# Kernel optimization log

Hardware: AMD Instinct MI355X
Metric: run time of the kernel (lower is better)

## Reference

```python
import jax, jax.numpy as jnp
import numpy as np

EPS = 1e-5

def _bn(x, s, b, m, v):
    # inference-mode BatchNorm2d over channel axis of NCHW
    return (x - m[None, :, None, None]) * jax.lax.rsqrt(v[None, :, None, None] + EPS) \
           * s[None, :, None, None] + b[None, :, None, None]

def _conv3(x, w):
    return jax.lax.conv_general_dilated(x, w, (1, 1), 'SAME',
                                        dimension_numbers=('NCHW', 'OIHW', 'NCHW'))

def _conv1(x, w, b):
    # 1x1 conv as einsum; w: [out_c, in_c]
    return jnp.einsum('oc,bchw->bohw', w, x) + b[None, :, None, None]

def _cca(f, qw, qb, kw, kb, vw, vb, gamma):
    # Criss-cross attention (faithful to source: no diagonal -inf masking, INF() unused there)
    B, C, H, W = f.shape
    q = _conv1(f, qw, qb)   # [B, C/8, H, W]
    k = _conv1(f, kw, kb)   # [B, C/8, H, W]
    v = _conv1(f, vw, vb)   # [B, C,   H, W]
    # energy along column (same w, all h') and row (same h, all w')
    eH = jnp.einsum('bchw,bciw->bhwi', q, k)            # [B,H,W,H]
    eW = jnp.einsum('bchw,bchj->bhwj', q, k)            # [B,H,W,W]
    att = jax.nn.softmax(jnp.concatenate([eH, eW], axis=3), axis=3)  # [B,H,W,H+W]
    aH, aW = att[..., :H], att[..., H:]
    oH = jnp.einsum('bhwi,bciw->bchw', aH, v)
    oW = jnp.einsum('bhwj,bchj->bchw', aW, v)
    return gamma * (oH + oW) + f


def setup_inputs() -> dict:
    key = jax.random.key(0)
    ks = iter(jax.random.split(key, 64))
    B, Cin, H, W = 8, 2048, 64, 64
    Ci, Cq, Co = 256, 32, 512
    rn = lambda s, sc=0.02: jax.random.normal(next(ks), s, jnp.float32) * sc
    ru = lambda s: jax.random.uniform(next(ks), s, jnp.float32)
    return {
        'x': jax.random.normal(next(ks), (B, Cin, H, W), jnp.float32),
        'recurrence': 2,
        'conva_w': rn((Ci, Cin, 3, 3)),
        'bn_a_s': ru((Ci,)), 'bn_a_b': rn((Ci,), 0.1), 'bn_a_m': rn((Ci,), 0.1), 'bn_a_v': ru((Ci,)),
        'q_w': rn((Cq, Ci)), 'q_b': rn((Cq,), 0.1),
        'k_w': rn((Cq, Ci)), 'k_b': rn((Cq,), 0.1),
        'v_w': rn((Ci, Ci)), 'v_b': rn((Ci,), 0.1),
        'cca_gamma': rn((1,), 1.0),
        'convb_w': rn((Ci, Ci, 3, 3)),
        'bn_b_s': ru((Ci,)), 'bn_b_b': rn((Ci,), 0.1), 'bn_b_m': rn((Ci,), 0.1), 'bn_b_v': ru((Ci,)),
        'sq_w': rn((Ci, Ci)), 'sq_b': rn((Ci,), 0.1),
        'bn_g_s': ru((Ci,)), 'bn_g_b': rn((Ci,), 0.1), 'bn_g_m': rn((Ci,), 0.1), 'bn_g_v': ru((Ci,)),
        'fc1_w': rn((Ci // 2, Ci)), 'fc1_b': rn((Ci // 2,), 0.1),
        'fc2_w': rn((Ci, Ci // 2)), 'fc2_b': rn((Ci,), 0.1),
        'bott_w': rn((Co, Cin + 2 * Ci, 3, 3)),
        'bn_t_s': ru((Co,)), 'bn_t_b': rn((Co,), 0.1), 'bn_t_m': rn((Co,), 0.1), 'bn_t_v': ru((Co,)),
    }


def reference(x, recurrence, conva_w, bn_a_s, bn_a_b, bn_a_m, bn_a_v,
              q_w, q_b, k_w, k_b, v_w, v_b, cca_gamma,
              convb_w, bn_b_s, bn_b_b, bn_b_m, bn_b_v,
              sq_w, sq_b, bn_g_s, bn_g_b, bn_g_m, bn_g_v,
              fc1_w, fc1_b, fc2_w, fc2_b,
              bott_w, bn_t_s, bn_t_b, bn_t_m, bn_t_v):
    out = _bn(_conv3(x, conva_w), bn_a_s, bn_a_b, bn_a_m, bn_a_v)
    # Global_Avg_Pooling (SE gating) on conva output
    fm = jax.nn.relu(_bn(_conv1(out, sq_w, sq_b), bn_g_s, bn_g_b, bn_g_m, bn_g_v))
    vec = fm.mean(axis=(-2, -1))                       # [B, Ci]
    h = jax.nn.relu(vec @ fc1_w.T + fc1_b)
    gate = jax.nn.sigmoid(h @ fc2_w.T + fc2_b)
    out_gap = out * gate[:, :, None, None]
    # recurrent criss-cross attention
    for _ in range(recurrence):
        out = _cca(out, q_w, q_b, k_w, k_b, v_w, v_b, cca_gamma)
    out = _bn(_conv3(out, convb_w), bn_b_s, bn_b_b, bn_b_m, bn_b_v)
    cat = jnp.concatenate([x, out, out_gap], axis=1)   # [B, Cin+2*Ci, H, W]
    return _bn(_conv3(cat, bott_w), bn_t_s, bn_t_b, bn_t_m, bn_t_v)
```

## Files before the change

kernel.cpp:

```cpp
#include <hip/hip_runtime.h>
#include <hip/hip_bf16.h>

typedef unsigned short u16;
typedef unsigned int u32;
typedef __attribute__((ext_vector_type(8))) short short8;
typedef __attribute__((ext_vector_type(8))) unsigned short u16x8;
typedef __attribute__((ext_vector_type(4))) float f32x4;

#define BN_EPS 1e-5f
#define PADW 66
#define CATC 2560

__device__ __forceinline__ u16 f2b(float f) {
    __hip_bfloat16 h = __float2bfloat16(f);
    return *reinterpret_cast<u16*>(&h);
}
__device__ __forceinline__ float b2f(u16 u) {
    __hip_bfloat16 h;
    *reinterpret_cast<u16*>(&h) = u;
    return __bfloat162float(h);
}
__device__ __forceinline__ void async_copy16(void* lds, const void* g) {
    __builtin_amdgcn_global_load_lds((const __attribute__((address_space(1))) u32*)g,
                                     (__attribute__((address_space(3))) u32*)lds, 16, 0, 0);
}
__device__ __forceinline__ void fence_() { asm volatile("" ::: "memory"); }
__device__ __forceinline__ void barrier_() { fence_(); __builtin_amdgcn_s_barrier(); fence_(); }

template<int TAPS, int BN, int EPI, int CPT, int NTILES, int KSPLIT>
__global__ __launch_bounds__(512, 2)
void gemm8(const u16* __restrict__ Ag, int cstride,
           const u16* __restrict__ Bg, int ktot_full, int klen,
           const float* __restrict__ alpha, const float* __restrict__ beta,
           u16* __restrict__ outb, int ostride, int ochoff,
           float* __restrict__ outf, int nch)
{
    constexpr int WN   = BN / 4;
    constexpr int NSUB = WN / 16;
    constexpr int NQ   = NSUB / 2;
    constexpr int BLH  = BN / 128;
    constexpr int ASZ  = 256 * 128;
    constexpr int BSZ  = BN * 128;
    const int KT = klen / 64;

    extern __shared__ __align__(16) char smem[];
    char* smA = smem;
    char* smB = smem + 2 * ASZ;

    const int tid  = threadIdx.x;
    const int lane = tid & 63;
    const int wave = tid >> 6;
    const int wr = wave >> 2;
    const int wc = wave & 3;

    const int nwg = gridDim.x;
    const int wg  = blockIdx.x;
    const int swz = (wg & 7) * (nwg >> 3) + (wg >> 3);
    const int sel = swz % (NTILES * KSPLIT);
    const int m0  = (swz / (NTILES * KSPLIT)) * 256;
    const int n0  = (sel / KSPLIT) * BN;
    const int ks  = sel % KSPLIT;
    const int kstart = ks * klen;

    const int sr = tid >> 3;
    const int sc = tid & 7;
    const int scx8 = (sc ^ (sr & 7)) * 8;
    long apix[4];
#pragma unroll
    for (int j = 0; j < 4; ++j) {
        int p = m0 + j * 64 + sr;
        int b = p >> 12, h = (p >> 6) & 63, w = p & 63;
        apix[j] = (TAPS == 1) ? ((long)(b * PADW + h + 1) * PADW + (w + 1))
                              : ((long)(b * PADW + h) * PADW + w);
    }
    long brow[2 * BLH];
#pragma unroll
    for (int h = 0; h < 2; ++h)
#pragma unroll
        for (int l = 0; l < BLH; ++l)
            brow[h * BLH + l] = (long)(n0 + h * (BN / 2) + l * 64 + sr) * ktot_full;

    auto stA = [&](int bsel, int h, int c0, long toff) {
#pragma unroll
        for (int l = 0; l < 2; ++l) {
            const u16* g = Ag + (apix[2 * h + l] + toff) * cstride + c0 + scx8;
            async_copy16(smA + bsel * ASZ + h * 16384 + l * 8192 + tid * 16, g);
        }
    };
    auto stB = [&](int bsel, int h, int k0) {
#pragma unroll
        for (int l = 0; l < BLH; ++l) {
            const u16* g = Bg + brow[h * BLH + l] + k0 + scx8;
            async_copy16(smB + bsel * BSZ + h * (BSZ / 2) + l * 8192 + tid * 16, g);
        }
    };

    const int rsel  = lane & 15;
    const int cswz0 = (((lane >> 4)     ^ (lane & 7)) << 4);
    const int cswz1 = (((4 | (lane >> 4)) ^ (lane & 7)) << 4);

    f32x4 acc[8][NSUB] = {};
    short8 a[4][2], b0[NQ][2], b1[NQ][2];

    auto ldA = [&](int bsel, int mh) {
        const char* base = smA + bsel * ASZ + (wr * 128 + mh * 64 + rsel) * 128;
#pragma unroll
        for (int mi = 0; mi < 4; ++mi) {
            a[mi][0] = *(const short8*)(base + mi * 2048 + cswz0);
            a[mi][1] = *(const short8*)(base + mi * 2048 + cswz1);
        }
    };
    auto ldB = [&](int bsel, int nh, short8 (&bb)[NQ][2]) {
        const char* base = smB + bsel * BSZ + (wc * WN + nh * (WN / 2) + rsel) * 128;
#pragma unroll
        for (int nj = 0; nj < NQ; ++nj) {
            bb[nj][0] = *(const short8*)(base + nj * 2048 + cswz0);
            bb[nj][1] = *(const short8*)(base + nj * 2048 + cswz1);
        }
    };
    auto quad = [&](int MH, int NH, short8 (&bb)[NQ][2]) {
#pragma unroll
        for (int mi = 0; mi < 4; ++mi)
#pragma unroll
            for (int nj = 0; nj < NQ; ++nj)
#pragma unroll
                for (int kk = 0; kk < 2; ++kk)
                    acc[MH * 4 + mi][NH * NQ + nj] =
                        __builtin_amdgcn_mfma_f32_16x16x32_bf16(
                            a[mi][kk], bb[nj][kk], acc[MH * 4 + mi][NH * NQ + nj], 0, 0, 0);
    };

    const int tap0 = kstart / CPT;
    int c0_ = kstart - tap0 * CPT;
    int dx_ = tap0 % 3;
    long toff_ = dx_ + (long)(tap0 / 3) * PADW;
    auto adv = [&]() {
        c0_ += 64;
        if (c0_ == CPT) { c0_ = 0; toff_ += 1; if (++dx_ == 3) { dx_ = 0; toff_ += PADW - 3; } }
    };

    stA(0, 0, c0_, toff_); stA(0, 1, c0_, toff_); stB(0, 0, kstart); stB(0, 1, kstart);
    adv();
    stB(1, 0, kstart + 64); stB(1, 1, kstart + 64); stA(1, 0, c0_, toff_); stA(1, 1, c0_, toff_);
    int pc0 = c0_; long ptoff = toff_;
    adv();
    int skb = kstart + 128;

    if constexpr (BN == 256) asm volatile("s_waitcnt vmcnt(8)" ::: "memory");
    else                     asm volatile("s_waitcnt vmcnt(6)" ::: "memory");
    barrier_();

    for (int kt = 0; kt < KT; ++kt) {
        const int buf = kt & 1;
        ldA(buf, 0); ldB(buf, 0, b0);
        if (kt >= 1 && kt + 1 < KT) stA(buf ^ 1, 1, pc0, ptoff);
        barrier_(); asm volatile("s_waitcnt lgkmcnt(0)" ::: "memory");
        __builtin_amdgcn_s_setprio(1); quad(0, 0, b0); __builtin_amdgcn_s_setprio(0);
        barrier_();
        ldB(buf, 1, b1);
        barrier_(); asm volatile("s_waitcnt lgkmcnt(0)" ::: "memory");
        __builtin_amdgcn_s_setprio(1); quad(0, 1, b1); __builtin_amdgcn_s_setprio(0);
        barrier_();
        ldA(buf, 1);
        if (kt + 2 < KT) stB(buf, 0, skb);
        barrier_(); asm volatile("s_waitcnt lgkmcnt(0)" ::: "memory");
        __builtin_amdgcn_s_setprio(1); quad(1, 0, b0); __builtin_amdgcn_s_setprio(0);
        barrier_();
        if (kt + 2 < KT) { stB(buf, 1, skb); stA(buf, 0, c0_, toff_); }
        barrier_();
        __builtin_amdgcn_s_setprio(1); quad(1, 1, b1); __builtin_amdgcn_s_setprio(0);
        if (kt + 2 >= KT) {
            asm volatile("s_waitcnt vmcnt(0)" ::: "memory");
        } else if constexpr (BN == 256) {
            asm volatile("s_waitcnt vmcnt(6)" ::: "memory");
        } else {
            asm volatile("s_waitcnt vmcnt(4)" ::: "memory");
        }
        barrier_();
        pc0 = c0_; ptoff = toff_;
        adv(); skb += 64;
    }

    const int nl = lane & 15, mq = lane >> 4;
#pragma unroll
    for (int s = 0; s < 8; ++s) {
#pragma unroll
        for (int nj = 0; nj < NSUB; ++nj) {
            int n = n0 + wc * WN + nj * 16 + nl;
            float al = (EPI == 4) ? 1.f : alpha[n];
            float be = (EPI == 4) ? 0.f : beta[n];
#pragma unroll
            for (int r = 0; r < 4; ++r) {
                int m = m0 + wr * 128 + s * 16 + mq * 4 + r;
                float v = acc[s][nj][r] * al + be;
                if (EPI == 0) {
                    int b = m >> 12, h = (m >> 6) & 63, w = m & 63;
                    long addr = ((long)(b * PADW + h + 1) * PADW + (w + 1)) * ostride + ochoff + n;
                    outb[addr] = f2b(v);
                } else if (EPI == 2) {
                    int b = m >> 12, h = (m >> 6) & 63, w = m & 63;
                    outf[((long)(b * nch + n) << 12) + (h * 64 + w)] = v;
                } else {
                    outf[(long)ks * ((long)32768 * nch) + (long)m * nch + n] = v;
                }
            }
        }
    }
}

__global__ void combine_k(const float* __restrict__ P,
                          const float* __restrict__ alpha, const float* __restrict__ beta,
                          u16* __restrict__ dst, int dstride, int choff)
{
    int m = blockIdx.x, n = threadIdx.x;
    int b = m >> 12, h = (m >> 6) & 63, w = m & 63;
    float v = P[(long)m * 256 + n] + P[(long)32768 * 256 + (long)m * 256 + n];
    v = v * alpha[n] + beta[n];
    dst[((long)(b * PADW + h + 1) * PADW + (w + 1)) * dstride + choff + n] = f2b(v);
}

template<int TAPS, int EPI>
__global__ __launch_bounds__(256, 2)
void gemm_conv(const u16* __restrict__ A, int cstride, int cpt,
               const u16* __restrict__ Bw, int ktot,
               const float* __restrict__ alpha, const float* __restrict__ beta,
               u16* __restrict__ outb, int ostride, int ochoff,
               float* __restrict__ outf, int n_total)
{
    __shared__ u16 As[128][32];
    __shared__ u16 Bs[128][32];
    __shared__ float red[128];

    const int tid  = threadIdx.x;
    const int lane = tid & 63;
    const int wave = tid >> 6;
    const int wr = wave >> 1, wc = wave & 1;
    const int m0 = blockIdx.y * 128;
    const int n0 = blockIdx.x * 128;

    long pixbase[2];
    long browk[2];
#pragma unroll
    for (int i = 0; i < 2; ++i) {
        int row = i * 64 + (tid >> 2);
        int p = m0 + row;
        int b = p >> 12, h = (p >> 6) & 63, w = p & 63;
        if (TAPS == 1) pixbase[i] = (long)(b * PADW + h + 1) * PADW + (w + 1);
        else           pixbase[i] = (long)(b * PADW + h) * PADW + w;
        browk[i] = (long)(n0 + row) * ktot;
    }
    const int chunk = (tid & 3) * 8;

    f32x4 acc[4][4] = {};

    const int steps = ktot / 32;
    int c0 = 0, dx = 0;
    long toff = 0;
    for (int s = 0; s < steps; ++s) {
        const int k0 = s * 32;
#pragma unroll
        for (int i = 0; i < 2; ++i) {
            const u16* ga = A + (pixbase[i] + ((TAPS == 1) ? 0 : toff)) * cstride + c0 + chunk;
            async_copy16((char*)(&As[0][0]) + i * 4096 + tid * 16, ga);
            const u16* gb = Bw + browk[i] + k0 + chunk;
            async_copy16((char*)(&Bs[0][0]) + i * 4096 + tid * 16, gb);
        }
        asm volatile("s_waitcnt vmcnt(0)" ::: "memory");
        __syncthreads();

        short8 af[4], bf[4];
#pragma unroll
        for (int x = 0; x < 4; ++x) {
            af[x] = *(const short8*)&As[wr * 64 + x * 16 + (lane & 15)][(lane >> 4) * 8];
            bf[x] = *(const short8*)&Bs[wc * 64 + x * 16 + (lane & 15)][(lane >> 4) * 8];
        }
#pragma unroll
        for (int mi = 0; mi < 4; ++mi)
#pragma unroll
            for (int ni = 0; ni < 4; ++ni)
                acc[mi][ni] = __builtin_amdgcn_mfma_f32_16x16x32_bf16(af[mi], bf[ni], acc[mi][ni], 0, 0, 0);
        __syncthreads();

        c0 += 32;
        if (TAPS > 1 && c0 == cpt) {
            c0 = 0; dx++; toff += 1;
            if (dx == 3) { dx = 0; toff += PADW - 3; }
        }
    }

    const int nl = lane & 15;
    const int mq = lane >> 4;

    if (EPI == 3) {
        if (tid < 128) red[tid] = 0.f;
        __syncthreads();
#pragma unroll
        for (int ni = 0; ni < 4; ++ni) {
            int ncol = wc * 64 + ni * 16 + nl;
            int n = n0 + ncol;
            float aa = alpha[n], bb = beta[n];
            float ssum = 0.f;
#pragma unroll
            for (int mi = 0; mi < 4; ++mi)
#pragma unroll
                for (int r = 0; r < 4; ++r)
                    ssum += fmaxf(acc[mi][ni][r] * aa + bb, 0.f);
            atomicAdd(&red[ncol], ssum);
        }
        __syncthreads();
        if (tid < 128) {
            int b = m0 >> 12;
            atomicAdd(&outf[b * 256 + n0 + tid], red[tid]);
        }
    } else {
#pragma unroll
        for (int mi = 0; mi < 4; ++mi) {
#pragma unroll
            for (int r = 0; r < 4; ++r) {
                int m = m0 + wr * 64 + mi * 16 + mq * 4 + r;
#pragma unroll
                for (int ni = 0; ni < 4; ++ni) {
                    int n = n0 + wc * 64 + ni * 16 + nl;
                    float v = acc[mi][ni][r] * alpha[n] + beta[n];
                    outb[(long)m * ostride + n] = f2b(v);
                }
            }
        }
    }
}

__global__ void xpad_k(const float* __restrict__ x, u16* __restrict__ cat)
{
    __shared__ float T[64][65];
    int bh = blockIdx.y;
    int b = bh >> 6, h = bh & 63;
    int c0 = blockIdx.x * 64;
    int t = threadIdx.x;
#pragma unroll
    for (int i = 0; i < 16; ++i) {
        int cl = i * 4 + (t >> 6);
        int w = t & 63;
        T[cl][w] = x[(((long)b * 2048 + c0 + cl) * 64 + h) * 64 + w];
    }
    __syncthreads();
#pragma unroll
    for (int i = 0; i < 16; ++i) {
        int wl = i * 4 + (t >> 6);
        int cl = t & 63;
        cat[((long)(b * PADW + h + 1) * PADW + (wl + 1)) * CATC + c0 + cl] = f2b(T[cl][wl]);
    }
}

__global__ void prep_w3(const float* __restrict__ w, u16* __restrict__ o, int O, int C)
{
    int idx = blockIdx.x * 256 + threadIdx.x;
    if (idx >= O * C) return;
    int oo = idx / C, c = idx - oo * C;
    const float* s = w + (long)idx * 9;
    long base = (long)oo * 9 * C + c;
#pragma unroll
    for (int t = 0; t < 9; ++t) o[base + (long)t * C] = f2b(s[t]);
}

__global__ void prep_qkv(const float* __restrict__ qw, const float* __restrict__ kw,
                         const float* __restrict__ vw, u16* __restrict__ o)
{
    int idx = blockIdx.x * 256 + threadIdx.x;
    int n = idx >> 8, c = idx & 255;
    float v;
    if (n < 32) v = qw[n * 256 + c];
    else if (n < 64) v = kw[(n - 32) * 256 + c];
    else if (n < 320) v = vw[(n - 64) * 256 + c];
    else v = 0.f;
    o[idx] = f2b(v);
}

__global__ void prep_cast(const float* __restrict__ w, u16* __restrict__ o, int n)
{
    int i = blockIdx.x * 256 + threadIdx.x;
    if (i < n) o[i] = f2b(w[i]);
}

__global__ void prep_ab(const float* as, const float* ab, const float* am, const float* av,
                        const float* gs, const float* gb, const float* gm, const float* gv, const float* sqb,
                        const float* bs, const float* bb, const float* bm, const float* bv,
                        const float* ts, const float* tb, const float* tm, const float* tv,
                        const float* qb, const float* kb, const float* vb,
                        float* Aa, float* Ba_, float* Ag, float* Bg, float* Ab2, float* Bb2,
                        float* At, float* Bt, float* Aq, float* Bq)
{
    int i = blockIdx.x * 256 + threadIdx.x;
    if (i < 256) { float al = as[i] * rsqrtf(av[i] + BN_EPS); Aa[i] = al; Ba_[i] = ab[i] - am[i] * al; }
    else if (i < 512) { int n = i - 256; float al = gs[n] * rsqrtf(gv[n] + BN_EPS); Ag[n] = al; Bg[n] = gb[n] - gm[n] * al + sqb[n] * al; }
    else if (i < 768) { int n = i - 512; float al = bs[n] * rsqrtf(bv[n] + BN_EPS); Ab2[n] = al; Bb2[n] = bb[n] - bm[n] * al; }
    else if (i < 1280) { int n = i - 768; float al = ts[n] * rsqrtf(tv[n] + BN_EPS); At[n] = al; Bt[n] = tb[n] - tm[n] * al; }
    else if (i < 1664) { int n = i - 1280; Aq[n] = 1.f; Bq[n] = (n < 32) ? qb[n] : (n < 64) ? kb[n - 32] : (n < 320) ? vb[n - 64] : 0.f; }
}

__global__ void gate_k(const float* __restrict__ vacc, const float* __restrict__ fc1w,
                       const float* __restrict__ fc1b, const float* __restrict__ fc2w,
                       const float* __restrict__ fc2b, float* __restrict__ gate)
{
    __shared__ float v[256], hbuf[128];
    int b = blockIdx.x, t = threadIdx.x;
    v[t] = vacc[b * 256 + t] * (1.f / 4096.f);
    __syncthreads();
    if (t < 128) {
        float s = fc1b[t];
        for (int c = 0; c < 256; ++c) s += v[c] * fc1w[t * 256 + c];
        hbuf[t] = fmaxf(s, 0.f);
    }
    __syncthreads();
    float s = fc2b[t];
    for (int j = 0; j < 128; ++j) s += hbuf[j] * fc2w[t * 128 + j];
    gate[b * 256 + t] = 1.f / (1.f + __expf(-s));
}

__global__ void gap_k(const u16* __restrict__ f0, const float* __restrict__ gate, u16* __restrict__ cat)
{
    int p = blockIdx.x, t = threadIdx.x;
    int b = p >> 12, h = (p >> 6) & 63, w = p & 63;
    long ppad = (long)(b * PADW + h + 1) * PADW + (w + 1);
    float f = b2f(f0[ppad * 256 + t]);
    cat[ppad * CATC + 2304 + t] = f2b(f * gate[b * 256 + t]);
}

__global__ void gram_k(const u16* __restrict__ qkv, float* __restrict__ e, int mode)
{
    __shared__ u16 Qs[64][32];
    __shared__ u16 Ks[64][32];
    int bx = blockIdx.x;
    int b = bx >> 6, s = bx & 63;
    int tid = threadIdx.x, lane = tid & 63, wave = tid >> 6;
    {
        int r = tid >> 2, ch = (tid & 3) * 8;
        long pix = (mode == 0) ? ((long)(b * 64 + r) * 64 + s) : ((long)(b * 64 + s) * 64 + r);
        const u16* g = qkv + pix * 384;
        *(u16x8*)&Qs[r][ch] = *(const u16x8*)(g + ch);
        *(u16x8*)&Ks[r][ch] = *(const u16x8*)(g + 32 + ch);
    }
    __syncthreads();
    f32x4 acc[4] = {};
    short8 a = *(const short8*)&Qs[wave * 16 + (lane & 15)][(lane >> 4) * 8];
#pragma unroll
    for (int ni = 0; ni < 4; ++ni) {
        short8 bb = *(const short8*)&Ks[ni * 16 + (lane & 15)][(lane >> 4) * 8];
        acc[ni] = __builtin_amdgcn_mfma_f32_16x16x32_bf16(a, bb, acc[ni], 0, 0, 0);
    }
#pragma unroll
    for (int ni = 0; ni < 4; ++ni)
#pragma unroll
        for (int r = 0; r < 4; ++r) {
            int row = wave * 16 + (lane >> 4) * 4 + r;
            int col = ni * 16 + (lane & 15);
            long pix = (mode == 0) ? ((long)(b * 64 + row) * 64 + s) : ((long)(b * 64 + s) * 64 + row);
            e[pix * 64 + col] = acc[ni][r];
        }
}

__global__ void softmax_k(const float* __restrict__ eH, const float* __restrict__ eW,
                          u16* __restrict__ aH, u16* __restrict__ aW)
{
    long row = blockIdx.x * 4 + (threadIdx.x >> 6);
    int lane = threadIdx.x & 63;
    float v0 = eH[row * 64 + lane];
    float v1 = eW[row * 64 + lane];
    float m = fmaxf(v0, v1);
#pragma unroll
    for (int off = 32; off; off >>= 1) m = fmaxf(m, __shfl_xor(m, off));
    float e0 = __expf(v0 - m), e1 = __expf(v1 - m);
    float s = e0 + e1;
#pragma unroll
    for (int off = 32; off; off >>= 1) s += __shfl_xor(s, off);
    float inv = 1.f / s;
    aH[row * 64 + lane] = f2b(e0 * inv);
    aW[row * 64 + lane] = f2b(e1 * inv);
}

__global__ __launch_bounds__(256, 2)
void oh_k(const u16* __restrict__ aH, const u16* __restrict__ qkv, float* __restrict__ oHb)
{
    __shared__ float Al[64][68];
    __shared__ u16 Vl[64][264];
    int bx = blockIdx.x;
    int b = bx >> 6, w = bx & 63;
    int t = threadIdx.x;
#pragma unroll
    for (int pass = 0; pass < 2; ++pass) {
        int r = pass * 32 + (t >> 3);
        int ch = (t & 7) * 8;
        u16x8 v = *(const u16x8*)(aH + ((long)(b * 64 + r) * 64 + w) * 64 + ch);
        f32x4 s0, s1;
#pragma unroll
        for (int u = 0; u < 4; ++u) { s0[u] = b2f(v[u]); s1[u] = b2f(v[4 + u]); }
        *(f32x4*)&Al[r][ch] = s0;
        *(f32x4*)&Al[r][ch + 4] = s1;
    }
#pragma unroll
    for (int pass = 0; pass < 8; ++pass) {
        int i = pass * 8 + (t >> 5);
        int ch = (t & 31) * 8;
        *(u16x8*)&Vl[i][ch] = *(const u16x8*)(qkv + ((long)(b * 64 + i) * 64 + w) * 384 + 64 + ch);
    }
    __syncthreads();
    int hb = (t >> 5) * 8, cb = (t & 31) * 8;
    float acc[8][8] = {};
    for (int i = 0; i < 64; ++i) {
        float av[8], vv[8];
        u16x8 v8 = *(const u16x8*)&Vl[i][cb];
#pragma unroll
        for (int u = 0; u < 8; ++u) av[u] = Al[hb + u][i];
#pragma unroll
        for (int u = 0; u < 8; ++u) vv[u] = b2f(v8[u]);
#pragma unroll
        for (int u = 0; u < 8; ++u)
#pragma unroll
            for (int x = 0; x < 8; ++x)
                acc[u][x] += av[u] * vv[x];
    }
#pragma unroll
    for (int u = 0; u < 8; ++u) {
        long base = ((long)(b * 64 + hb + u) * 64 + w) * 256 + cb;
        f32x4 s0, s1;
#pragma unroll
        for (int x = 0; x < 4; ++x) { s0[x] = acc[u][x]; s1[x] = acc[u][4 + x]; }
        *(f32x4*)&oHb[base] = s0;
        *(f32x4*)&oHb[base + 4] = s1;
    }
}

__global__ __launch_bounds__(256, 2)
void ow_k(const u16* __restrict__ aW, const u16* __restrict__ qkv, const float* __restrict__ oHb,
          const u16* __restrict__ fin, u16* __restrict__ fout, const float* __restrict__ gamma_p)
{
    __shared__ float Al[64][68];
    __shared__ u16 Vl[64][264];
    int bx = blockIdx.x;
    int b = bx >> 6, h = bx & 63;
    int t = threadIdx.x;
    float gamma = gamma_p[0];
#pragma unroll
    for (int pass = 0; pass < 2; ++pass) {
        int r = pass * 32 + (t >> 3);
        int ch = (t & 7) * 8;
        u16x8 v = *(const u16x8*)(aW + ((long)(b * 64 + h) * 64 + r) * 64 + ch);
        f32x4 s0, s1;
#pragma unroll
        for (int u = 0; u < 4; ++u) { s0[u] = b2f(v[u]); s1[u] = b2f(v[4 + u]); }
        *(f32x4*)&Al[r][ch] = s0;
        *(f32x4*)&Al[r][ch + 4] = s1;
    }
#pragma unroll
    for (int pass = 0; pass < 8; ++pass) {
        int j = pass * 8 + (t >> 5);
        int ch = (t & 31) * 8;
        *(u16x8*)&Vl[j][ch] = *(const u16x8*)(qkv + ((long)(b * 64 + h) * 64 + j) * 384 + 64 + ch);
    }
    __syncthreads();
    int wb = (t >> 5) * 8, cb = (t & 31) * 8;
    float acc[8][8] = {};
    for (int j = 0; j < 64; ++j) {
        float av[8], vv[8];
        u16x8 v8 = *(const u16x8*)&Vl[j][cb];
#pragma unroll
        for (int u = 0; u < 8; ++u) av[u] = Al[wb + u][j];
#pragma unroll
        for (int u = 0; u < 8; ++u) vv[u] = b2f(v8[u]);
#pragma unroll
        for (int u = 0; u < 8; ++u)
#pragma unroll
            for (int x = 0; x < 8; ++x)
                acc[u][x] += av[u] * vv[x];
    }
#pragma unroll
    for (int u = 0; u < 8; ++u) {
        int w = wb + u;
        long pix = ((long)(b * 64 + h) * 64 + w) * 256 + cb;
        long pp = ((long)(b * PADW + h + 1) * PADW + (w + 1)) * 256 + cb;
        u16x8 f8 = *(const u16x8*)&fin[pp];
        f32x4 o0 = *(const f32x4*)&oHb[pix];
        f32x4 o1 = *(const f32x4*)&oHb[pix + 4];
        u16x8 r8;
#pragma unroll
        for (int x = 0; x < 8; ++x) {
            float o = acc[u][x] + ((x < 4) ? o0[x] : o1[x - 4]);
            r8[x] = f2b(gamma * o + b2f(f8[x]));
        }
        *(u16x8*)&fout[pp] = r8;
    }
}

extern "C" void kernel_launch(void* const* d_in, const int* in_sizes, int n_in,
                              void* d_out, int out_size, void* d_ws, size_t ws_size,
                              hipStream_t stream)
{
    const float* x       = (const float*)d_in[0];
    const float* conva_w = (const float*)d_in[2];
    const float* bn_a_s  = (const float*)d_in[3];
    const float* bn_a_b  = (const float*)d_in[4];
    const float* bn_a_m  = (const float*)d_in[5];
    const float* bn_a_v  = (const float*)d_in[6];
    const float* q_w     = (const float*)d_in[7];
    const float* q_b     = (const float*)d_in[8];
    const float* k_w     = (const float*)d_in[9];
    const float* k_b     = (const float*)d_in[10];
    const float* v_w     = (const float*)d_in[11];
    const float* v_b     = (const float*)d_in[12];
    const float* gamma   = (const float*)d_in[13];
    const float* convb_w = (const float*)d_in[14];
    const float* bn_b_s  = (const float*)d_in[15];
    const float* bn_b_b  = (const float*)d_in[16];
    const float* bn_b_m  = (const float*)d_in[17];
    const float* bn_b_v  = (const float*)d_in[18];
    const float* sq_w    = (const float*)d_in[19];
    const float* sq_b    = (const float*)d_in[20];
    const float* bn_g_s  = (const float*)d_in[21];
    const float* bn_g_b  = (const float*)d_in[22];
    const float* bn_g_m  = (const float*)d_in[23];
    const float* bn_g_v  = (const float*)d_in[24];
    const float* fc1_w   = (const float*)d_in[25];
    const float* fc1_b   = (const float*)d_in[26];
    const float* fc2_w   = (const float*)d_in[27];
    const float* fc2_b   = (const float*)d_in[28];
    const float* bott_w  = (const float*)d_in[29];
    const float* bn_t_s  = (const float*)d_in[30];
    const float* bn_t_b  = (const float*)d_in[31];
    const float* bn_t_m  = (const float*)d_in[32];
    const float* bn_t_v  = (const float*)d_in[33];

    char* ws = (char*)d_ws;
    size_t off = 0;
    auto alloc = [&](size_t bytes) { char* p = ws + off; off += (bytes + 255) & ~(size_t)255; return p; };

    u16*   CAT  = (u16*)  alloc((size_t)8 * PADW * PADW * CATC * 2);
    u16*   F0   = (u16*)  alloc((size_t)8 * PADW * PADW * 256 * 2);
    u16*   F1   = (u16*)  alloc((size_t)8 * PADW * PADW * 256 * 2);
    size_t cca_off = off;
    u16*   QKV  = (u16*)  alloc((size_t)32768 * 384 * 2);
    float* EH   = (float*)alloc((size_t)32768 * 64 * 4);
    float* EWb  = (float*)alloc((size_t)32768 * 64 * 4);
    u16*   AH   = (u16*)  alloc((size_t)32768 * 64 * 2);
    u16*   AW   = (u16*)  alloc((size_t)32768 * 64 * 2);
    float* OHB  = (float*)alloc((size_t)32768 * 256 * 4);
    float* P    = (float*)(ws + cca_off);
    u16*   WA   = (u16*)  alloc((size_t)256 * 18432 * 2);
    u16*   WB   = (u16*)  alloc((size_t)256 * 2304 * 2);
    u16*   WT   = (u16*)  alloc((size_t)512 * 23040 * 2);
    u16*   WQKV = (u16*)  alloc((size_t)384 * 256 * 2);
    u16*   WSQ  = (u16*)  alloc((size_t)256 * 256 * 2);
    float* Aa   = (float*)alloc(256 * 4);
    float* Ba_  = (float*)alloc(256 * 4);
    float* Ag   = (float*)alloc(256 * 4);
    float* Bg   = (float*)alloc(256 * 4);
    float* Ab2  = (float*)alloc(256 * 4);
    float* Bb2  = (float*)alloc(256 * 4);
    float* At   = (float*)alloc(512 * 4);
    float* Bt   = (float*)alloc(512 * 4);
    float* Aq   = (float*)alloc(384 * 4);
    float* Bq   = (float*)alloc(384 * 4);
    float* VACC = (float*)alloc(8 * 256 * 4);
    float* GATE = (float*)alloc(8 * 256 * 4);

    hipFuncSetAttribute((const void*)gemm8<9, 256, 4, 2048, 1, 2>,
                        hipFuncAttributeMaxDynamicSharedMemorySize, 131072);
    hipFuncSetAttribute((const void*)gemm8<9, 256, 4, 256, 1, 2>,
                        hipFuncAttributeMaxDynamicSharedMemorySize, 131072);
    hipFuncSetAttribute((const void*)gemm8<9, 256, 2, 2560, 2, 1>,
                        hipFuncAttributeMaxDynamicSharedMemorySize, 131072);

    hipMemsetAsync(CAT, 0, (size_t)8 * PADW * PADW * CATC * 2, stream);
    hipMemsetAsync(F0, 0, (size_t)2 * 8 * PADW * PADW * 256 * 2, stream);
    hipMemsetAsync(VACC, 0, 8 * 256 * 4, stream);

    prep_w3<<<(256 * 2048 + 255) / 256, 256, 0, stream>>>(conva_w, WA, 256, 2048);
    prep_w3<<<(256 * 256 + 255) / 256, 256, 0, stream>>>(convb_w, WB, 256, 256);
    prep_w3<<<(512 * 2560 + 255) / 256, 256, 0, stream>>>(bott_w, WT, 512, 2560);
    prep_qkv<<<384, 256, 0, stream>>>(q_w, k_w, v_w, WQKV);
    prep_cast<<<256, 256, 0, stream>>>(sq_w, WSQ, 65536);
    prep_ab<<<7, 256, 0, stream>>>(bn_a_s, bn_a_b, bn_a_m, bn_a_v,
                                   bn_g_s, bn_g_b, bn_g_m, bn_g_v, sq_b,
                                   bn_b_s, bn_b_b, bn_b_m, bn_b_v,
                                   bn_t_s, bn_t_b, bn_t_m, bn_t_v,
                                   q_b, k_b, v_b,
                                   Aa, Ba_, Ag, Bg, Ab2, Bb2, At, Bt, Aq, Bq);
    xpad_k<<<dim3(32, 512), 256, 0, stream>>>(x, CAT);

    gemm8<9, 256, 4, 2048, 1, 2><<<256, 512, 131072, stream>>>(
        CAT, CATC, WA, 18432, 9216, Aa, Ba_, nullptr, 0, 0, P, 256);
    combine_k<<<32768, 256, 0, stream>>>(P, Aa, Ba_, F0, 256, 0);

    gemm_conv<1, 3><<<dim3(2, 256), 256, 0, stream>>>(F0, 256, 256, WSQ, 256, Ag, Bg, nullptr, 0, 0, VACC, 0);
    gate_k<<<8, 256, 0, stream>>>(VACC, fc1_w, fc1_b, fc2_w, fc2_b, GATE);
    gap_k<<<32768, 256, 0, stream>>>(F0, GATE, CAT);

    for (int rec = 0; rec < 2; ++rec) {
        u16* fin = rec ? F1 : F0;
        u16* fout = rec ? F0 : F1;
        gemm_conv<1, 1><<<dim3(3, 256), 256, 0, stream>>>(fin, 256, 256, WQKV, 256, Aq, Bq, QKV, 384, 0, nullptr, 0);
        gram_k<<<512, 256, 0, stream>>>(QKV, EH, 0);
        gram_k<<<512, 256, 0, stream>>>(QKV, EWb, 1);
        softmax_k<<<8192, 256, 0, stream>>>(EH, EWb, AH, AW);
        oh_k<<<512, 256, 0, stream>>>(AH, QKV, OHB);
        ow_k<<<512, 256, 0, stream>>>(AW, QKV, OHB, fin, fout, gamma);
    }

    gemm8<9, 256, 4, 256, 1, 2><<<256, 512, 131072, stream>>>(
        F0, 256, WB, 2304, 1152, Ab2, Bb2, nullptr, 0, 0, P, 256);
    combine_k<<<32768, 256, 0, stream>>>(P, Ab2, Bb2, CAT, CATC, 2048);

    gemm8<9, 256, 2, 2560, 2, 1><<<256, 512, 131072, stream>>>(
        CAT, CATC, WT, 23040, 23040, At, Bt, nullptr, 0, 0, (float*)d_out, 512);
}
```

Baseline: 1.315 ms.

## Zero only padded borders, vectorize combine, merge gram launches, precompute A offsets

Replaces the full-buffer memsets of the padded CAT and F0 tensors with a kernel that zeroes only the one-pixel border, which removes roughly a hundred megabytes of redundant writes. The split-K combine kernel now handles four channels per thread with vector loads and stores. The two gram launches are merged into a single launch, and the GEMM's A-address arithmetic is folded into precomputed element offsets so the inner loop does less index math. The border-only zeroing depends on every interior pixel being fully overwritten, and F1's border is left unzeroed, so this relies on F1's border never being read.

```diff
diff --git a/kernel.cpp b/kernel.cpp
--- a/kernel.cpp
+++ b/kernel.cpp
@@ -5,6 +5,7 @@
 typedef unsigned int u32;
 typedef __attribute__((ext_vector_type(8))) short short8;
 typedef __attribute__((ext_vector_type(8))) unsigned short u16x8;
+typedef __attribute__((ext_vector_type(4))) unsigned short u16x4;
 typedef __attribute__((ext_vector_type(4))) float f32x4;
 
 #define BN_EPS 1e-5f
@@ -65,32 +66,33 @@
     const int sr = tid >> 3;
     const int sc = tid & 7;
     const int scx8 = (sc ^ (sr & 7)) * 8;
-    long apix[4];
+    long baseAe[4];
 #pragma unroll
     for (int j = 0; j < 4; ++j) {
         int p = m0 + j * 64 + sr;
         int b = p >> 12, h = (p >> 6) & 63, w = p & 63;
-        apix[j] = (TAPS == 1) ? ((long)(b * PADW + h + 1) * PADW + (w + 1))
-                              : ((long)(b * PADW + h) * PADW + w);
-    }
-    long brow[2 * BLH];
+        long apix = (TAPS == 1) ? ((long)(b * PADW + h + 1) * PADW + (w + 1))
+                                : ((long)(b * PADW + h) * PADW + w);
+        baseAe[j] = apix * cstride + scx8;
+    }
+    long baseBe[2 * BLH];
 #pragma unroll
     for (int h = 0; h < 2; ++h)
 #pragma unroll
         for (int l = 0; l < BLH; ++l)
-            brow[h * BLH + l] = (long)(n0 + h * (BN / 2) + l * 64 + sr) * ktot_full;
-
-    auto stA = [&](int bsel, int h, int c0, long toff) {
+            baseBe[h * BLH + l] = (long)(n0 + h * (BN / 2) + l * 64 + sr) * ktot_full + scx8;
+
+    auto stA = [&](int bsel, int h, long aoff) {
 #pragma unroll
         for (int l = 0; l < 2; ++l) {
-            const u16* g = Ag + (apix[2 * h + l] + toff) * cstride + c0 + scx8;
+            const u16* g = Ag + baseAe[2 * h + l] + aoff;
             async_copy16(smA + bsel * ASZ + h * 16384 + l * 8192 + tid * 16, g);
         }
     };
     auto stB = [&](int bsel, int h, int k0) {
 #pragma unroll
         for (int l = 0; l < BLH; ++l) {
-            const u16* g = Bg + brow[h * BLH + l] + k0 + scx8;
+            const u16* g = Bg + baseBe[h * BLH + l] + k0;
             async_copy16(smB + bsel * BSZ + h * (BSZ / 2) + l * 8192 + tid * 16, g);
         }
     };
@@ -133,16 +135,19 @@
     const int tap0 = kstart / CPT;
     int c0_ = kstart - tap0 * CPT;
     int dx_ = tap0 % 3;
-    long toff_ = dx_ + (long)(tap0 / 3) * PADW;
+    long aoff_ = ((long)dx_ + (long)(tap0 / 3) * PADW) * cstride + c0_;
     auto adv = [&]() {
-        c0_ += 64;
-        if (c0_ == CPT) { c0_ = 0; toff_ += 1; if (++dx_ == 3) { dx_ = 0; toff_ += PADW - 3; } }
+        c0_ += 64; aoff_ += 64;
+        if (c0_ == CPT) {
+            c0_ = 0; aoff_ += (long)cstride - CPT;
+            if (++dx_ == 3) { dx_ = 0; aoff_ += (long)(PADW - 3) * cstride; }
+        }
     };
 
-    stA(0, 0, c0_, toff_); stA(0, 1, c0_, toff_); stB(0, 0, kstart); stB(0, 1, kstart);
+    stA(0, 0, aoff_); stA(0, 1, aoff_); stB(0, 0, kstart); stB(0, 1, kstart);
     adv();
-    stB(1, 0, kstart + 64); stB(1, 1, kstart + 64); stA(1, 0, c0_, toff_); stA(1, 1, c0_, toff_);
-    int pc0 = c0_; long ptoff = toff_;
+    stB(1, 0, kstart + 64); stB(1, 1, kstart + 64); stA(1, 0, aoff_); stA(1, 1, aoff_);
+    long paoff = aoff_;
     adv();
     int skb = kstart + 128;
 
@@ -153,7 +158,7 @@
     for (int kt = 0; kt < KT; ++kt) {
         const int buf = kt & 1;
         ldA(buf, 0); ldB(buf, 0, b0);
-        if (kt >= 1 && kt + 1 < KT) stA(buf ^ 1, 1, pc0, ptoff);
+        if (kt >= 1 && kt + 1 < KT) stA(buf ^ 1, 1, paoff);
         barrier_(); asm volatile("s_waitcnt lgkmcnt(0)" ::: "memory");
         __builtin_amdgcn_s_setprio(1); quad(0, 0, b0); __builtin_amdgcn_s_setprio(0);
         barrier_();
@@ -166,7 +171,7 @@
         barrier_(); asm volatile("s_waitcnt lgkmcnt(0)" ::: "memory");
         __builtin_amdgcn_s_setprio(1); quad(1, 0, b0); __builtin_amdgcn_s_setprio(0);
         barrier_();
-        if (kt + 2 < KT) { stB(buf, 1, skb); stA(buf, 0, c0_, toff_); }
+        if (kt + 2 < KT) { stB(buf, 1, skb); stA(buf, 0, aoff_); }
         barrier_();
         __builtin_amdgcn_s_setprio(1); quad(1, 1, b1); __builtin_amdgcn_s_setprio(0);
         if (kt + 2 >= KT) {
@@ -177,7 +182,7 @@
             asm volatile("s_waitcnt vmcnt(4)" ::: "memory");
         }
         barrier_();
-        pc0 = c0_; ptoff = toff_;
+        paoff = aoff_;
         adv(); skb += 64;
     }
 
@@ -212,11 +217,35 @@
                           const float* __restrict__ alpha, const float* __restrict__ beta,
                           u16* __restrict__ dst, int dstride, int choff)
 {
-    int m = blockIdx.x, n = threadIdx.x;
+    int t = threadIdx.x;
+    int m = blockIdx.x * 4 + (t >> 6);
+    int n = (t & 63) * 4;
     int b = m >> 12, h = (m >> 6) & 63, w = m & 63;
-    float v = P[(long)m * 256 + n] + P[(long)32768 * 256 + (long)m * 256 + n];
-    v = v * alpha[n] + beta[n];
-    dst[((long)(b * PADW + h + 1) * PADW + (w + 1)) * dstride + choff + n] = f2b(v);
+    f32x4 v0 = *(const f32x4*)&P[(long)m * 256 + n];
+    f32x4 v1 = *(const f32x4*)&P[(long)32768 * 256 + (long)m * 256 + n];
+    f32x4 al = *(const f32x4*)&alpha[n];
+    f32x4 be = *(const f32x4*)&beta[n];
+    u16x4 r;
+#pragma unroll
+    for (int i = 0; i < 4; ++i) r[i] = f2b((v0[i] + v1[i]) * al[i] + be[i]);
+    *(u16x4*)&dst[((long)(b * PADW + h + 1) * PADW + (w + 1)) * dstride + choff + n] = r;
+}
+
+__global__ void border_k(u16* __restrict__ cat, u16* __restrict__ f0)
+{
+    int i = blockIdx.x;
+    int b = i / 260, r = i - b * 260;
+    int ph, pw;
+    if (r < 66)       { ph = 0;        pw = r; }
+    else if (r < 132) { ph = 65;       pw = r - 66; }
+    else if (r < 196) { ph = r - 131;  pw = 0; }
+    else              { ph = r - 195;  pw = 65; }
+    long pix = (long)(b * PADW + ph) * PADW + pw;
+    int t = threadIdx.x;
+    u16x8 z = {};
+    *(u16x8*)&cat[pix * CATC + t * 8] = z;
+    if (t < 64) *(u16x8*)&cat[pix * CATC + 2048 + t * 8] = z;
+    if (t < 32) *(u16x8*)&f0[pix * 256 + t * 8] = z;
 }
 
 template<int TAPS, int EPI>
@@ -425,19 +454,22 @@
     cat[ppad * CATC + 2304 + t] = f2b(f * gate[b * 256 + t]);
 }
 
-__global__ void gram_k(const u16* __restrict__ qkv, float* __restrict__ e, int mode)
+__global__ void gram_k(const u16* __restrict__ qkv, float* eH, float* eW)
 {
     __shared__ u16 Qs[64][32];
     __shared__ u16 Ks[64][32];
-    int bx = blockIdx.x;
+    int g = blockIdx.x;
+    int mode = g >> 9;
+    int bx = g & 511;
     int b = bx >> 6, s = bx & 63;
+    float* e = mode ? eW : eH;
     int tid = threadIdx.x, lane = tid & 63, wave = tid >> 6;
     {
         int r = tid >> 2, ch = (tid & 3) * 8;
         long pix = (mode == 0) ? ((long)(b * 64 + r) * 64 + s) : ((long)(b * 64 + s) * 64 + r);
-        const u16* g = qkv + pix * 384;
-        *(u16x8*)&Qs[r][ch] = *(const u16x8*)(g + ch);
-        *(u16x8*)&Ks[r][ch] = *(const u16x8*)(g + 32 + ch);
+        const u16* gp = qkv + pix * 384;
+        *(u16x8*)&Qs[r][ch] = *(const u16x8*)(gp + ch);
+        *(u16x8*)&Ks[r][ch] = *(const u16x8*)(gp + 32 + ch);
     }
     __syncthreads();
     f32x4 acc[4] = {};
@@ -668,10 +700,9 @@
     hipFuncSetAttribute((const void*)gemm8<9, 256, 2, 2560, 2, 1>,
                         hipFuncAttributeMaxDynamicSharedMemorySize, 131072);
 
-    hipMemsetAsync(CAT, 0, (size_t)8 * PADW * PADW * CATC * 2, stream);
-    hipMemsetAsync(F0, 0, (size_t)2 * 8 * PADW * PADW * 256 * 2, stream);
     hipMemsetAsync(VACC, 0, 8 * 256 * 4, stream);
 
+    border_k<<<8 * 260, 256, 0, stream>>>(CAT, F0);
     prep_w3<<<(256 * 2048 + 255) / 256, 256, 0, stream>>>(conva_w, WA, 256, 2048);
     prep_w3<<<(256 * 256 + 255) / 256, 256, 0, stream>>>(convb_w, WB, 256, 256);
     prep_w3<<<(512 * 2560 + 255) / 256, 256, 0, stream>>>(bott_w, WT, 512, 2560);
@@ -687,7 +718,7 @@
 
     gemm8<9, 256, 4, 2048, 1, 2><<<256, 512, 131072, stream>>>(
         CAT, CATC, WA, 18432, 9216, Aa, Ba_, nullptr, 0, 0, P, 256);
-    combine_k<<<32768, 256, 0, stream>>>(P, Aa, Ba_, F0, 256, 0);
+    combine_k<<<8192, 256, 0, stream>>>(P, Aa, Ba_, F0, 256, 0);
 
     gemm_conv<1, 3><<<dim3(2, 256), 256, 0, stream>>>(F0, 256, 256, WSQ, 256, Ag, Bg, nullptr, 0, 0, VACC, 0);
     gate_k<<<8, 256, 0, stream>>>(VACC, fc1_w, fc1_b, fc2_w, fc2_b, GATE);
@@ -697,8 +728,7 @@
         u16* fin = rec ? F1 : F0;
         u16* fout = rec ? F0 : F1;
         gemm_conv<1, 1><<<dim3(3, 256), 256, 0, stream>>>(fin, 256, 256, WQKV, 256, Aq, Bq, QKV, 384, 0, nullptr, 0);
-        gram_k<<<512, 256, 0, stream>>>(QKV, EH, 0);
-        gram_k<<<512, 256, 0, stream>>>(QKV, EWb, 1);
+        gram_k<<<1024, 256, 0, stream>>>(QKV, EH, EWb);
         softmax_k<<<8192, 256, 0, stream>>>(EH, EWb, AH, AW);
         oh_k<<<512, 256, 0, stream>>>(AH, QKV, OHB);
         ow_k<<<512, 256, 0, stream>>>(AW, QKV, OHB, fin, fout, gamma);
@@ -706,7 +736,7 @@
 
     gemm8<9, 256, 4, 256, 1, 2><<<256, 512, 131072, stream>>>(
         F0, 256, WB, 2304, 1152, Ab2, Bb2, nullptr, 0, 0, P, 256);
-    combine_k<<<32768, 256, 0, stream>>>(P, Ab2, Bb2, CAT, CATC, 2048);
+    combine_k<<<8192, 256, 0, stream>>>(P, Ab2, Bb2, CAT, CATC, 2048);
 
     gemm8<9, 256, 2, 2560, 2, 1><<<256, 512, 131072, stream>>>(
         CAT, CATC, WT, 23040, 23040, At, Bt, nullptr, 0, 0, (float*)d_out, 512);
```

Measured after the change: 1.232 ms. 6.3% less time.
